# Kernel optimization log

Measured on AMD Instinct MI355X. Metric: run time of the kernel, lower is better.

Reference implementation:

```python
import jax, jax.numpy as jnp
import numpy as np

RADIUS = 64
STRIDE = RADIUS // 2
EPS = 1e-5

def box_filter(x, w):
    # depthwise conv: groups=3, RADIUSxRADIUS kernel of ones, stride RADIUS//2, no padding
    return jax.lax.conv_general_dilated(
        x, w, window_strides=(STRIDE, STRIDE), padding='VALID',
        feature_group_count=3, dimension_numbers=('NCHW', 'OIHW', 'NCHW'))

def conv1x1(x, w):
    # 1x1 conv == per-pixel matmul over channels
    return jnp.einsum('bchw,oc->bohw', x, w)

def batchnorm(x, g, b):
    # BatchNorm2d in training mode: biased batch stats over (N,H,W)
    m = jnp.mean(x, axis=(0, 2, 3), keepdims=True)
    v = jnp.var(x, axis=(0, 2, 3), keepdims=True)
    return (x - m) * jax.lax.rsqrt(v + EPS) * g[None, :, None, None] + b[None, :, None, None]

def resize_bilinear_ac(x, oh, ow):
    # F.interpolate(mode='bilinear', align_corners=True), separable gathers
    B, C, h, w = x.shape
    ys = jnp.linspace(0.0, h - 1.0, oh)
    y0 = jnp.floor(ys).astype(jnp.int32)
    y1 = jnp.minimum(y0 + 1, h - 1)
    wy = (ys - y0.astype(x.dtype))[None, None, :, None]
    xh = jnp.take(x, y0, axis=2) * (1 - wy) + jnp.take(x, y1, axis=2) * wy
    xs = jnp.linspace(0.0, w - 1.0, ow)
    x0 = jnp.floor(xs).astype(jnp.int32)
    x1 = jnp.minimum(x0 + 1, w - 1)
    wx = (xs - x0.astype(x.dtype))[None, None, None, :]
    return jnp.take(xh, x0, axis=3) * (1 - wx) + jnp.take(xh, x1, axis=3) * wx

def setup_inputs():
    key = jax.random.key(0)
    ks = jax.random.split(key, 5)
    B, H, W = 4, 1024, 1024
    guide = jax.random.uniform(ks[0], (B, 3, H, W), dtype=jnp.float32)
    src = jax.random.uniform(ks[1], (B, 3, H, W), dtype=jnp.float32)
    box_w = jnp.ones((3, 1, RADIUS, RADIUS), jnp.float32)  # weight.data[...] = 1.0
    w1 = jax.random.normal(ks[2], (32, 6), jnp.float32) * 0.2
    w2 = jax.random.normal(ks[3], (32, 32), jnp.float32) * 0.2
    w3 = jax.random.normal(ks[4], (3, 32), jnp.float32) * 0.2
    g1 = jnp.ones((32,), jnp.float32); b1 = jnp.zeros((32,), jnp.float32)
    g2 = jnp.ones((32,), jnp.float32); b2 = jnp.zeros((32,), jnp.float32)
    return dict(guide=guide, src=src, box_w=box_w, w1=w1, g1=g1, b1=b1,
                w2=w2, g2=g2, b2=b2, w3=w3)

def reference(guide, src, box_w, w1, g1, b1, w2, g2, b2, w3):
    B, C, H, W = guide.shape
    N = box_filter(jnp.ones((1, 3, H, W), guide.dtype), box_w)  # local window counts
    mean_x = box_filter(guide, box_w) / N
    mean_y = box_filter(src, box_w) / N
    cov_xy = box_filter(guide * src, box_w) / N - mean_x * mean_y
    var_x = box_filter(guide * guide, box_w) / N - mean_x * mean_x
    h = jnp.concatenate([cov_xy, var_x], axis=1)  # [B,6,h',w']
    h = jax.nn.relu(batchnorm(conv1x1(h, w1), g1, b1))
    h = jax.nn.relu(batchnorm(conv1x1(h, w2), g2, b2))
    A = conv1x1(h, w3)  # [B,3,h',w']
    b = mean_y - A * mean_x
    mean_A = resize_bilinear_ac(A, H, W)
    mean_b = resize_bilinear_ac(b, H, W)
    return mean_A * guide + mean_b
```

## Files before the change

kernel.cpp:

```cpp
#include <hip/hip_runtime.h>
#include <stdint.h>

#define B_      4
#define C_      3
#define H_      1024
#define W_      1024
#define OH_     31
#define NHS_    64
#define NP_     3844
#define NPOSPB_ 961
#define EPS_    1e-5f

#define NBLK_    256
#define NTHR_    768
#define MIDBLK_  21
#define NSHARD_  8
#define SHARD_TGT_ 32
#define LINE_    32

#define TILE_PLANE 24576
#define OFF_TILE  0
#define OFF_STATS 98304
#define OFF_A     98432
#define OFF_BV    109964

typedef float f4 __attribute__((ext_vector_type(4)));

__device__ int g_shard[2][NSHARD_ * LINE_];
__device__ int g_root[2][LINE_];
__device__ int g_bn1[2][LINE_];
__device__ int g_bn2[2][LINE_];
__device__ int g_done[2][LINE_];
__device__ int g_parity;

static __device__ __forceinline__ int  rload(int* p) { return __hip_atomic_load(p, __ATOMIC_RELAXED, __HIP_MEMORY_SCOPE_AGENT); }
static __device__ __forceinline__ int  aacq(int* p)  { return __hip_atomic_load(p, __ATOMIC_ACQUIRE, __HIP_MEMORY_SCOPE_AGENT); }
static __device__ __forceinline__ int  aadd(int* p, int v) { return __hip_atomic_fetch_add(p, v, __ATOMIC_ACQ_REL, __HIP_MEMORY_SCOPE_AGENT); }
static __device__ __forceinline__ void astoref(float* p, float v) { __hip_atomic_store(p, v, __ATOMIC_RELAXED, __HIP_MEMORY_SCOPE_AGENT); }
static __device__ __forceinline__ void astorei(int* p, int v)     { __hip_atomic_store(p, v, __ATOMIC_RELAXED, __HIP_MEMORY_SCOPE_AGENT); }
static __device__ __forceinline__ float aloadf(float* p) { return __hip_atomic_load(p, __ATOMIC_RELAXED, __HIP_MEMORY_SCOPE_AGENT); }

#define SPIN(ctr, target, slp) do { \
    if (t == 0) { \
        while (rload(ctr) < (target)) __builtin_amdgcn_s_sleep(slp); \
        (void)aacq(ctr);    \
    } \
    __syncthreads(); \
} while (0)

__global__ __launch_bounds__(NTHR_) void fused(
        const float* __restrict__ g,
        const float* __restrict__ s,
        const float* __restrict__ w1f,
        const float* __restrict__ g1f,
        const float* __restrict__ b1f,
        const float* __restrict__ w2f,
        const float* __restrict__ g2f,
        const float* __restrict__ b2f,
        const float* __restrict__ w3f,
        float* __restrict__ ws,
        float* __restrict__ out) {
    __shared__ float zbuf[192 * 33];
    __shared__ float red[12][16];
    __shared__ float scs[32], shs[32];
    __shared__ int sP;
    int t  = threadIdx.x;
    int fb = blockIdx.x;
    if (t == 0) sP = __hip_atomic_load(&g_parity, __ATOMIC_RELAXED, __HIP_MEMORY_SCOPE_AGENT);

    {
        int sub = t >> 8;
        int st  = t & 255;
        int unit = fb * 3 + sub;
        int bc = unit >> 6;
        int hs = unit & 63;
        const f4* gp = (const f4*)(g + ((size_t)bc * H_ + (size_t)hs * 16) * W_);
        const f4* sp = (const f4*)(s + ((size_t)bc * H_ + (size_t)hs * 16) * W_);
        float sg = 0.f, ss = 0.f, sgs = 0.f, sgg = 0.f;
#pragma unroll 4
        for (int r = 0; r < 16; r++) {
            f4 gv = gp[r * (W_ / 4) + st];
            f4 sv = __builtin_nontemporal_load(sp + r * (W_ / 4) + st);
            sg  += (gv.x + gv.y) + (gv.z + gv.w);
            ss  += (sv.x + sv.y) + (sv.z + sv.w);
            sgs += gv.x * sv.x + gv.y * sv.y + gv.z * sv.z + gv.w * sv.w;
            sgg += gv.x * gv.x + gv.y * gv.y + gv.z * gv.z + gv.w * gv.w;
        }
#pragma unroll
        for (int off = 4; off; off >>= 1) {
            sg  += __shfl_down(sg,  off, 8);
            ss  += __shfl_down(ss,  off, 8);
            sgs += __shfl_down(sgs, off, 8);
            sgg += __shfl_down(sgg, off, 8);
        }
        if ((st & 7) == 0) {
            int tx = st >> 3;
            int base = (bc * NHS_ + hs) * 32 + tx;
            astoref(&ws[OFF_TILE + 0 * TILE_PLANE + base], sg);
            astoref(&ws[OFF_TILE + 1 * TILE_PLANE + base], ss);
            astoref(&ws[OFF_TILE + 2 * TILE_PLANE + base], sgs);
            astoref(&ws[OFF_TILE + 3 * TILE_PLANE + base], sgg);
        }
        if (fb == 0 && t < 128) astoref(&ws[OFF_STATS + t], 0.f);
    }
    __syncthreads();
    int P = sP;

    if (t == 0) {
        int sh = fb & (NSHARD_ - 1);
        int old = aadd(&g_shard[P][sh * LINE_], 1);
        if (old == SHARD_TGT_ - 1) aadd(&g_root[P][0], 1);
    }

    if (fb < MIDBLK_) {
        SPIN(&g_root[P][0], NSHARD_, 2);

        int w    = t >> 6;
        int lane = t & 63;
        int k    = w & 3;
        int ko8  = __builtin_amdgcn_readfirstlane(k * 8);
        int pl   = (w >> 2) * 64 + lane;
        int p    = fb * 192 + pl;
        bool ok  = p < NP_;
        int pp   = ok ? p : 0;
        int b    = pp / NPOSPB_;
        int r    = pp % NPOSPB_;
        int oy   = r / OH_, ox = r % OH_;

        float h[6], mxv[3], myv[3];
#pragma unroll
        for (int c = 0; c < 3; c++) {
            int bc = b * 3 + c;
            int base = (bc * NHS_ + oy * 2) * 32 + ox;
            float S[4];
#pragma unroll
            for (int plane = 0; plane < 4; plane++) {
                const float* tp = ws + OFF_TILE + plane * TILE_PLANE + base;
                S[plane] = ((tp[0]  + tp[1])  + (tp[32] + tp[33]))
                         + ((tp[64] + tp[65]) + (tp[96] + tp[97]));
            }
            const float inv = 1.f / 4096.f;
            float mx = S[0] * inv, my = S[1] * inv;
            h[c]     = S[2] * inv - mx * my;
            h[3 + c] = S[3] * inv - mx * mx;
            mxv[c] = mx; myv[c] = my;
        }
        float a[8];
#pragma unroll
        for (int j = 0; j < 8; j++) {
            float y = 0.f;
#pragma unroll
            for (int i = 0; i < 6; i++) y += w1f[(ko8 + j) * 6 + i] * h[i];
            a[j] = y;
        }

        {
            float sv[8], sq[8];
#pragma unroll
            for (int j = 0; j < 8; j++) { sv[j] = ok ? a[j] : 0.f; sq[j] = sv[j] * sv[j]; }
#pragma unroll
            for (int off = 32; off; off >>= 1) {
#pragma unroll
                for (int j = 0; j < 8; j++) {
                    sv[j] += __shfl_down(sv[j], off, 64);
                    sq[j] += __shfl_down(sq[j], off, 64);
                }
            }
            if (lane == 0) {
#pragma unroll
                for (int j = 0; j < 8; j++) { red[w][j] = sv[j]; red[w][8 + j] = sq[j]; }
            }
        }
        __syncthreads();
        if (t < 64) {
            int o = t & 31; int kk = o >> 3; int col = ((t >= 32) ? 8 : 0) + (o & 7);
            float tot = red[kk][col] + red[kk + 4][col] + red[kk + 8][col];
            atomicAdd(&ws[OFF_STATS + ((t >= 32) ? 32 : 0) + o], tot);
        }
        __syncthreads();
        if (t == 0) aadd(&g_bn1[P][0], 1);
        SPIN(&g_bn1[P][0], MIDBLK_, 2);

        if (t < 32) {
            float sm = aloadf(&ws[OFF_STATS + t]);
            float sq = aloadf(&ws[OFF_STATS + 32 + t]);
            float m = sm * (1.f / NP_);
            float v = sq * (1.f / NP_) - m * m;
            float sc = g1f[t] * rsqrtf(v + EPS_);
            scs[t] = sc; shs[t] = b1f[t] - m * sc;
        }
        __syncthreads();

#pragma unroll
        for (int j = 0; j < 8; j++) {
            float zz = fmaxf(a[j] * scs[ko8 + j] + shs[ko8 + j], 0.f);
            zbuf[pl * 33 + ko8 + j] = zz;
        }
        __syncthreads();
        float zal[32];
#pragma unroll
        for (int i = 0; i < 32; i++) zal[i] = zbuf[pl * 33 + i];
        float y2[8];
#pragma unroll
        for (int j = 0; j < 8; j++) {
            float y = 0.f;
#pragma unroll
            for (int i = 0; i < 32; i++) y += w2f[(ko8 + j) * 32 + i] * zal[i];
            y2[j] = y;
        }

        {
            float sv[8], sq[8];
#pragma unroll
            for (int j = 0; j < 8; j++) { sv[j] = ok ? y2[j] : 0.f; sq[j] = sv[j] * sv[j]; }
#pragma unroll
            for (int off = 32; off; off >>= 1) {
#pragma unroll
                for (int j = 0; j < 8; j++) {
                    sv[j] += __shfl_down(sv[j], off, 64);
                    sq[j] += __shfl_down(sq[j], off, 64);
                }
            }
            if (lane == 0) {
#pragma unroll
                for (int j = 0; j < 8; j++) { red[w][j] = sv[j]; red[w][8 + j] = sq[j]; }
            }
        }
        __syncthreads();
        if (t < 64) {
            int o = t & 31; int kk = o >> 3; int col = ((t >= 32) ? 8 : 0) + (o & 7);
            float tot = red[kk][col] + red[kk + 4][col] + red[kk + 8][col];
            atomicAdd(&ws[OFF_STATS + 64 + ((t >= 32) ? 32 : 0) + o], tot);
        }
        __syncthreads();
        if (t == 0) aadd(&g_bn2[P][0], 1);
        SPIN(&g_bn2[P][0], MIDBLK_, 2);

        if (t < 32) {
            float sm = aloadf(&ws[OFF_STATS + 64 + t]);
            float sq = aloadf(&ws[OFF_STATS + 96 + t]);
            float m = sm * (1.f / NP_);
            float v = sq * (1.f / NP_) - m * m;
            float sc = g2f[t] * rsqrtf(v + EPS_);
            scs[t] = sc; shs[t] = b2f[t] - m * sc;
        }
        __syncthreads();

#pragma unroll
        for (int j = 0; j < 8; j++) {
            float zz = fmaxf(y2[j] * scs[ko8 + j] + shs[ko8 + j], 0.f);
            zbuf[pl * 33 + ko8 + j] = zz;
        }
        __syncthreads();
        if (k == 0 && ok) {
            float z2[32];
#pragma unroll
            for (int i = 0; i < 32; i++) z2[i] = zbuf[pl * 33 + i];
#pragma unroll
            for (int c = 0; c < 3; c++) {
                float av = 0.f;
#pragma unroll
                for (int i = 0; i < 32; i++) av += w3f[c * 32 + i] * z2[i];
                astoref(&ws[OFF_A  + c * NP_ + p], av);
                astoref(&ws[OFF_BV + c * NP_ + p], myv[c] - av * mxv[c]);
            }
        }
        __syncthreads();
        if (t == 0) {
            int old = aadd(&g_done[P][0], 1);
            if (old == MIDBLK_ - 1) {
                int Q = P ^ 1;
#pragma unroll
                for (int i = 0; i < NSHARD_; i++) astorei(&g_shard[Q][i * LINE_], 0);
                astorei(&g_root[Q][0], 0);
                astorei(&g_bn1[Q][0], 0);
                astorei(&g_bn2[Q][0], 0);
                astorei(&g_done[Q][0], 0);
                __hip_atomic_store(&g_parity, Q, __ATOMIC_RELEASE, __HIP_MEMORY_SCOPE_AGENT);
            }
        }
    }

    SPIN(&g_done[P][0], MIDBLK_, 32);

    {
        int sub = t >> 8;
        int st  = t & 255;
        int row0 = fb * 48 + sub * 16;
        int bc = row0 >> 10;
        int b5 = bc / 3, c5 = bc % 3;
        const float* Abase = ws + OFF_A  + c5 * NP_ + b5 * NPOSPB_;
        const float* Bbase = ws + OFF_BV + c5 * NP_ + b5 * NPOSPB_;
        int x0_[4], x1_[4]; float wx_[4];
#pragma unroll
        for (int j = 0; j < 4; j++) {
            int x = st * 4 + j;
            float fx = (float)x * (30.f / 1023.f);
            int x0 = (int)fx;
            wx_[j] = fx - (float)x0;
            x0_[j] = x0;
            x1_[j] = min(x0 + 1, 30);
        }
        for (int rr = 0; rr < 16; rr++) {
            int y = (row0 & 1023) + rr;
            float fy = (float)y * (30.f / 1023.f);
            int y0 = (int)fy;
            float wy = fy - (float)y0;
            int y1i = min(y0 + 1, 30);
            const float* A0 = Abase + y0  * OH_;
            const float* A1 = Abase + y1i * OH_;
            const float* B0 = Bbase + y0  * OH_;
            const float* B1 = Bbase + y1i * OH_;
            size_t rowoff = ((size_t)bc * H_ + (size_t)y) * W_;
            f4 gv = ((const f4*)(g + rowoff))[st];
            float go[4] = { gv.x, gv.y, gv.z, gv.w };
            float r[4];
#pragma unroll
            for (int j = 0; j < 4; j++) {
                int x0 = x0_[j], x1 = x1_[j];
                float wx = wx_[j];
                float av = (A0[x0] * (1.f - wx) + A0[x1] * wx) * (1.f - wy)
                         + (A1[x0] * (1.f - wx) + A1[x1] * wx) * wy;
                float bb = (B0[x0] * (1.f - wx) + B0[x1] * wx) * (1.f - wy)
                         + (B1[x0] * (1.f - wx) + B1[x1] * wx) * wy;
                r[j] = av * go[j] + bb;
            }
            f4 ov; ov.x = r[0]; ov.y = r[1]; ov.z = r[2]; ov.w = r[3];
            __builtin_nontemporal_store(ov, (f4*)(out + rowoff) + st);
        }
    }
}

extern "C" void kernel_launch(void* const* d_in, const int* in_sizes, int n_in,
                              void* d_out, int out_size, void* d_ws, size_t ws_size,
                              hipStream_t stream) {
    const float* guide = (const float*)d_in[0];
    const float* src   = (const float*)d_in[1];
    const float* w1 = (const float*)d_in[3];
    const float* g1 = (const float*)d_in[4];
    const float* b1 = (const float*)d_in[5];
    const float* w2 = (const float*)d_in[6];
    const float* g2 = (const float*)d_in[7];
    const float* b2 = (const float*)d_in[8];
    const float* w3 = (const float*)d_in[9];
    float* ws = (float*)d_ws;
    float* out = (float*)d_out;

    hipLaunchKernelGGL(fused, dim3(NBLK_), dim3(NTHR_), 0, stream,
                       guide, src, w1, g1, b1, w2, g2, b2, w3, ws, out);
}
```

Baseline: 191.6 us.

## Spread MLP/BN stage across all blocks and keep guide tile in registers

The middle MLP/batchnorm stage, previously done by 21 blocks while the other blocks spun, is now split across all 256 blocks at 16 positions each. Weights are staged in LDS, and BN statistics go to 8 shadow slots to reduce atomic contention. Every barrier now uses the sharded arrive/root scheme. Each thread keeps its 16 guide rows in registers from the first pass and reuses them in the final output pass, removing the second read of guide. The cost is more grid-wide barriers touching all blocks and higher register pressure from holding 16 float4 values.

```diff
diff --git a/kernel.cpp b/kernel.cpp
--- a/kernel.cpp
+++ b/kernel.cpp
@@ -13,24 +13,23 @@
 
 #define NBLK_    256
 #define NTHR_    768
-#define MIDBLK_  21
 #define NSHARD_  8
 #define SHARD_TGT_ 32
 #define LINE_    32
+#define NSHADOW_ 8
 
 #define TILE_PLANE 24576
 #define OFF_TILE  0
 #define OFF_STATS 98304
-#define OFF_A     98432
-#define OFF_BV    109964
+#define OFF_A     99328
+#define OFF_BV    110860
 
 typedef float f4 __attribute__((ext_vector_type(4)));
 
-__device__ int g_shard[2][NSHARD_ * LINE_];
-__device__ int g_root[2][LINE_];
-__device__ int g_bn1[2][LINE_];
-__device__ int g_bn2[2][LINE_];
-__device__ int g_done[2][LINE_];
+__device__ int g_b0s[2][NSHARD_ * LINE_]; __device__ int g_b0r[2][LINE_];
+__device__ int g_b1s[2][NSHARD_ * LINE_]; __device__ int g_b1r[2][LINE_];
+__device__ int g_b2s[2][NSHARD_ * LINE_]; __device__ int g_b2r[2][LINE_];
+__device__ int g_b3s[2][NSHARD_ * LINE_]; __device__ int g_b3r[2][LINE_];
 __device__ int g_parity;
 
 static __device__ __forceinline__ int  rload(int* p) { return __hip_atomic_load(p, __ATOMIC_RELAXED, __HIP_MEMORY_SCOPE_AGENT); }
@@ -40,10 +39,16 @@
 static __device__ __forceinline__ void astorei(int* p, int v)     { __hip_atomic_store(p, v, __ATOMIC_RELAXED, __HIP_MEMORY_SCOPE_AGENT); }
 static __device__ __forceinline__ float aloadf(float* p) { return __hip_atomic_load(p, __ATOMIC_RELAXED, __HIP_MEMORY_SCOPE_AGENT); }
 
-#define SPIN(ctr, target, slp) do { \
+#define ARRIVE(shard, root) do { \
     if (t == 0) { \
-        while (rload(ctr) < (target)) __builtin_amdgcn_s_sleep(slp); \
-        (void)aacq(ctr);    \
+        int _o = aadd(&(shard)[(fb & (NSHARD_ - 1)) * LINE_], 1); \
+        if (_o == SHARD_TGT_ - 1) aadd(&(root)[0], 1); \
+    } \
+} while (0)
+#define SPINROOT(root, slp) do { \
+    if (t == 0) { \
+        while (rload(&(root)[0]) < NSHARD_) __builtin_amdgcn_s_sleep(slp); \
+        (void)aacq(&(root)[0]); \
     } \
     __syncthreads(); \
 } while (0)
@@ -60,27 +65,38 @@
         const float* __restrict__ w3f,
         float* __restrict__ ws,
         float* __restrict__ out) {
-    __shared__ float zbuf[192 * 33];
-    __shared__ float red[12][16];
+    __shared__ float w1L[192];
+    __shared__ float w2L[32 * 33];
+    __shared__ float w3L[3 * 33];
+    __shared__ float Sarr[16][12];
+    __shared__ float hbuf[16][8];
+    __shared__ float mxb[16][4], myb[16][4];
+    __shared__ float sbuf[16][33];
+    __shared__ float zbuf[16][33];
     __shared__ float scs[32], shs[32];
     __shared__ int sP;
     int t  = threadIdx.x;
     int fb = blockIdx.x;
-    if (t == 0) sP = __hip_atomic_load(&g_parity, __ATOMIC_RELAXED, __HIP_MEMORY_SCOPE_AGENT);
-
+    if (t == 0) sP = rload(&g_parity);
+
+    if (t < 192) w1L[t] = w1f[t];
+    for (int i = t; i < 1024; i += NTHR_) w2L[(i >> 5) * 33 + (i & 31)] = w2f[i];
+    if (t < 96) w3L[(t >> 5) * 33 + (t & 31)] = w3f[t];
+
+    int sub = t >> 8;
+    int st  = t & 255;
+    f4 gvals[16];
     {
-        int sub = t >> 8;
-        int st  = t & 255;
         int unit = fb * 3 + sub;
-        int bc = unit >> 6;
-        int hs = unit & 63;
-        const f4* gp = (const f4*)(g + ((size_t)bc * H_ + (size_t)hs * 16) * W_);
-        const f4* sp = (const f4*)(s + ((size_t)bc * H_ + (size_t)hs * 16) * W_);
+        int ibc = unit >> 6, hs = unit & 63;
+        const f4* gp = (const f4*)(g + ((size_t)ibc * H_ + (size_t)hs * 16) * W_);
+        const f4* sp = (const f4*)(s + ((size_t)ibc * H_ + (size_t)hs * 16) * W_);
         float sg = 0.f, ss = 0.f, sgs = 0.f, sgg = 0.f;
-#pragma unroll 4
+#pragma unroll
         for (int r = 0; r < 16; r++) {
-            f4 gv = gp[r * (W_ / 4) + st];
+            f4 gv = __builtin_nontemporal_load(gp + r * (W_ / 4) + st);
             f4 sv = __builtin_nontemporal_load(sp + r * (W_ / 4) + st);
+            gvals[r] = gv;
             sg  += (gv.x + gv.y) + (gv.z + gv.w);
             ss  += (sv.x + sv.y) + (sv.z + sv.w);
             sgs += gv.x * sv.x + gv.y * sv.y + gv.z * sv.z + gv.w * sv.w;
@@ -95,197 +111,140 @@
         }
         if ((st & 7) == 0) {
             int tx = st >> 3;
-            int base = (bc * NHS_ + hs) * 32 + tx;
+            int base = (ibc * NHS_ + hs) * 32 + tx;
             astoref(&ws[OFF_TILE + 0 * TILE_PLANE + base], sg);
             astoref(&ws[OFF_TILE + 1 * TILE_PLANE + base], ss);
             astoref(&ws[OFF_TILE + 2 * TILE_PLANE + base], sgs);
             astoref(&ws[OFF_TILE + 3 * TILE_PLANE + base], sgg);
         }
-        if (fb == 0 && t < 128) astoref(&ws[OFF_STATS + t], 0.f);
+        if (fb == 0) for (int i = t; i < NSHADOW_ * 128; i += NTHR_) astoref(&ws[OFF_STATS + i], 0.f);
     }
     __syncthreads();
     int P = sP;
-
+    ARRIVE(g_b0s[P], g_b0r[P]);
+
+    SPINROOT(g_b0r[P], 2);
+
+    int p0 = fb * 16;
+    if (t < 192) {
+        int ipos = t / 12, idx = t % 12;
+        int c = idx >> 2, plane = idx & 3;
+        int p = p0 + ipos; if (p >= NP_) p = 0;
+        int b = p / NPOSPB_, r = p % NPOSPB_;
+        int oy = r / OH_, ox = r % OH_;
+        const float* tp = ws + OFF_TILE + plane * TILE_PLANE + ((b * 3 + c) * NHS_ + oy * 2) * 32 + ox;
+        Sarr[ipos][idx] = ((tp[0]  + tp[1])  + (tp[32] + tp[33]))
+                        + ((tp[64] + tp[65]) + (tp[96] + tp[97]));
+    }
+    __syncthreads();
+    if (t < 48) {
+        int pos = t / 3, c = t % 3;
+        const float inv = 1.f / 4096.f;
+        float mx = Sarr[pos][c * 4 + 0] * inv, my = Sarr[pos][c * 4 + 1] * inv;
+        hbuf[pos][c]     = Sarr[pos][c * 4 + 2] * inv - mx * my;
+        hbuf[pos][3 + c] = Sarr[pos][c * 4 + 3] * inv - mx * mx;
+        mxb[pos][c] = mx; myb[pos][c] = my;
+    }
+    __syncthreads();
+    int pos = t >> 5, ch = t & 31;
+    bool act = t < 512;
+    bool valid = act && (p0 + pos) < NP_;
+    float y1 = 0.f;
+    if (act) {
+#pragma unroll
+        for (int i = 0; i < 6; i++) y1 += w1L[ch * 6 + i] * hbuf[pos][i];
+        sbuf[pos][ch] = valid ? y1 : 0.f;
+    }
+    __syncthreads();
+    if (t < 32) {
+        float sv = 0.f, sq = 0.f;
+#pragma unroll
+        for (int i = 0; i < 16; i++) { float v = sbuf[i][t]; sv += v; sq += v * v; }
+        float* sh0 = ws + OFF_STATS + (fb & (NSHADOW_ - 1)) * 128;
+        atomicAdd(&sh0[t], sv); atomicAdd(&sh0[32 + t], sq);
+    }
+    __syncthreads();
+    ARRIVE(g_b1s[P], g_b1r[P]);
+    SPINROOT(g_b1r[P], 2);
+    if (t < 32) {
+        float sm = 0.f, sq = 0.f;
+#pragma unroll
+        for (int k = 0; k < NSHADOW_; k++) {
+            sm += aloadf(&ws[OFF_STATS + k * 128 + t]);
+            sq += aloadf(&ws[OFF_STATS + k * 128 + 32 + t]);
+        }
+        float m = sm * (1.f / NP_);
+        float v = sq * (1.f / NP_) - m * m;
+        float sc = g1f[t] * rsqrtf(v + EPS_);
+        scs[t] = sc; shs[t] = b1f[t] - m * sc;
+    }
+    __syncthreads();
+    if (act) zbuf[pos][ch] = fmaxf(y1 * scs[ch] + shs[ch], 0.f);
+    __syncthreads();
+    float y2 = 0.f;
+    if (act) {
+#pragma unroll
+        for (int i = 0; i < 32; i++) y2 += w2L[ch * 33 + i] * zbuf[pos][i];
+        sbuf[pos][ch] = valid ? y2 : 0.f;
+    }
+    __syncthreads();
+    if (t < 32) {
+        float sv = 0.f, sq = 0.f;
+#pragma unroll
+        for (int i = 0; i < 16; i++) { float v = sbuf[i][t]; sv += v; sq += v * v; }
+        float* sh0 = ws + OFF_STATS + (fb & (NSHADOW_ - 1)) * 128;
+        atomicAdd(&sh0[64 + t], sv); atomicAdd(&sh0[96 + t], sq);
+    }
+    __syncthreads();
+    ARRIVE(g_b2s[P], g_b2r[P]);
+    SPINROOT(g_b2r[P], 2);
+    if (t < 32) {
+        float sm = 0.f, sq = 0.f;
+#pragma unroll
+        for (int k = 0; k < NSHADOW_; k++) {
+            sm += aloadf(&ws[OFF_STATS + k * 128 + 64 + t]);
+            sq += aloadf(&ws[OFF_STATS + k * 128 + 96 + t]);
+        }
+        float m = sm * (1.f / NP_);
+        float v = sq * (1.f / NP_) - m * m;
+        float sc = g2f[t] * rsqrtf(v + EPS_);
+        scs[t] = sc; shs[t] = b2f[t] - m * sc;
+    }
+    __syncthreads();
+    if (act) zbuf[pos][ch] = fmaxf(y2 * scs[ch] + shs[ch], 0.f);
+    __syncthreads();
+    if (t < 48) {
+        int pz = t / 3, c = t % 3;
+        int p = p0 + pz;
+        if (p < NP_) {
+            float A = 0.f;
+#pragma unroll
+            for (int i = 0; i < 32; i++) A += w3L[c * 33 + i] * zbuf[pz][i];
+            astoref(&ws[OFF_A  + c * NP_ + p], A);
+            astoref(&ws[OFF_BV + c * NP_ + p], myb[pz][c] - A * mxb[pz][c]);
+        }
+    }
+    __syncthreads();
     if (t == 0) {
-        int sh = fb & (NSHARD_ - 1);
-        int old = aadd(&g_shard[P][sh * LINE_], 1);
-        if (old == SHARD_TGT_ - 1) aadd(&g_root[P][0], 1);
-    }
-
-    if (fb < MIDBLK_) {
-        SPIN(&g_root[P][0], NSHARD_, 2);
-
-        int w    = t >> 6;
-        int lane = t & 63;
-        int k    = w & 3;
-        int ko8  = __builtin_amdgcn_readfirstlane(k * 8);
-        int pl   = (w >> 2) * 64 + lane;
-        int p    = fb * 192 + pl;
-        bool ok  = p < NP_;
-        int pp   = ok ? p : 0;
-        int b    = pp / NPOSPB_;
-        int r    = pp % NPOSPB_;
-        int oy   = r / OH_, ox = r % OH_;
-
-        float h[6], mxv[3], myv[3];
-#pragma unroll
-        for (int c = 0; c < 3; c++) {
-            int bc = b * 3 + c;
-            int base = (bc * NHS_ + oy * 2) * 32 + ox;
-            float S[4];
-#pragma unroll
-            for (int plane = 0; plane < 4; plane++) {
-                const float* tp = ws + OFF_TILE + plane * TILE_PLANE + base;
-                S[plane] = ((tp[0]  + tp[1])  + (tp[32] + tp[33]))
-                         + ((tp[64] + tp[65]) + (tp[96] + tp[97]));
-            }
-            const float inv = 1.f / 4096.f;
-            float mx = S[0] * inv, my = S[1] * inv;
-            h[c]     = S[2] * inv - mx * my;
-            h[3 + c] = S[3] * inv - mx * mx;
-            mxv[c] = mx; myv[c] = my;
-        }
-        float a[8];
-#pragma unroll
-        for (int j = 0; j < 8; j++) {
-            float y = 0.f;
-#pragma unroll
-            for (int i = 0; i < 6; i++) y += w1f[(ko8 + j) * 6 + i] * h[i];
-            a[j] = y;
-        }
-
-        {
-            float sv[8], sq[8];
-#pragma unroll
-            for (int j = 0; j < 8; j++) { sv[j] = ok ? a[j] : 0.f; sq[j] = sv[j] * sv[j]; }
-#pragma unroll
-            for (int off = 32; off; off >>= 1) {
-#pragma unroll
-                for (int j = 0; j < 8; j++) {
-                    sv[j] += __shfl_down(sv[j], off, 64);
-                    sq[j] += __shfl_down(sq[j], off, 64);
+        int old = aadd(&g_b3s[P][(fb & (NSHARD_ - 1)) * LINE_], 1);
+        if (old == SHARD_TGT_ - 1) {
+            int ro = aadd(&g_b3r[P][0], 1);
+            if (ro == NSHARD_ - 1) {
+                int Q = P ^ 1;
+#pragma unroll
+                for (int i = 0; i < NSHARD_; i++) {
+                    astorei(&g_b0s[Q][i * LINE_], 0); astorei(&g_b1s[Q][i * LINE_], 0);
+                    astorei(&g_b2s[Q][i * LINE_], 0); astorei(&g_b3s[Q][i * LINE_], 0);
                 }
-            }
-            if (lane == 0) {
-#pragma unroll
-                for (int j = 0; j < 8; j++) { red[w][j] = sv[j]; red[w][8 + j] = sq[j]; }
-            }
-        }
-        __syncthreads();
-        if (t < 64) {
-            int o = t & 31; int kk = o >> 3; int col = ((t >= 32) ? 8 : 0) + (o & 7);
-            float tot = red[kk][col] + red[kk + 4][col] + red[kk + 8][col];
-            atomicAdd(&ws[OFF_STATS + ((t >= 32) ? 32 : 0) + o], tot);
-        }
-        __syncthreads();
-        if (t == 0) aadd(&g_bn1[P][0], 1);
-        SPIN(&g_bn1[P][0], MIDBLK_, 2);
-
-        if (t < 32) {
-            float sm = aloadf(&ws[OFF_STATS + t]);
-            float sq = aloadf(&ws[OFF_STATS + 32 + t]);
-            float m = sm * (1.f / NP_);
-            float v = sq * (1.f / NP_) - m * m;
-            float sc = g1f[t] * rsqrtf(v + EPS_);
-            scs[t] = sc; shs[t] = b1f[t] - m * sc;
-        }
-        __syncthreads();
-
-#pragma unroll
-        for (int j = 0; j < 8; j++) {
-            float zz = fmaxf(a[j] * scs[ko8 + j] + shs[ko8 + j], 0.f);
-            zbuf[pl * 33 + ko8 + j] = zz;
-        }
-        __syncthreads();
-        float zal[32];
-#pragma unroll
-        for (int i = 0; i < 32; i++) zal[i] = zbuf[pl * 33 + i];
-        float y2[8];
-#pragma unroll
-        for (int j = 0; j < 8; j++) {
-            float y = 0.f;
-#pragma unroll
-            for (int i = 0; i < 32; i++) y += w2f[(ko8 + j) * 32 + i] * zal[i];
-            y2[j] = y;
-        }
-
-        {
-            float sv[8], sq[8];
-#pragma unroll
-            for (int j = 0; j < 8; j++) { sv[j] = ok ? y2[j] : 0.f; sq[j] = sv[j] * sv[j]; }
-#pragma unroll
-            for (int off = 32; off; off >>= 1) {
-#pragma unroll
-                for (int j = 0; j < 8; j++) {
-                    sv[j] += __shfl_down(sv[j], off, 64);
-                    sq[j] += __shfl_down(sq[j], off, 64);
-                }
-            }
-            if (lane == 0) {
-#pragma unroll
-                for (int j = 0; j < 8; j++) { red[w][j] = sv[j]; red[w][8 + j] = sq[j]; }
-            }
-        }
-        __syncthreads();
-        if (t < 64) {
-            int o = t & 31; int kk = o >> 3; int col = ((t >= 32) ? 8 : 0) + (o & 7);
-            float tot = red[kk][col] + red[kk + 4][col] + red[kk + 8][col];
-            atomicAdd(&ws[OFF_STATS + 64 + ((t >= 32) ? 32 : 0) + o], tot);
-        }
-        __syncthreads();
-        if (t == 0) aadd(&g_bn2[P][0], 1);
-        SPIN(&g_bn2[P][0], MIDBLK_, 2);
-
-        if (t < 32) {
-            float sm = aloadf(&ws[OFF_STATS + 64 + t]);
-            float sq = aloadf(&ws[OFF_STATS + 96 + t]);
-            float m = sm * (1.f / NP_);
-            float v = sq * (1.f / NP_) - m * m;
-            float sc = g2f[t] * rsqrtf(v + EPS_);
-            scs[t] = sc; shs[t] = b2f[t] - m * sc;
-        }
-        __syncthreads();
-
-#pragma unroll
-        for (int j = 0; j < 8; j++) {
-            float zz = fmaxf(y2[j] * scs[ko8 + j] + shs[ko8 + j], 0.f);
-            zbuf[pl * 33 + ko8 + j] = zz;
-        }
-        __syncthreads();
-        if (k == 0 && ok) {
-            float z2[32];
-#pragma unroll
-            for (int i = 0; i < 32; i++) z2[i] = zbuf[pl * 33 + i];
-#pragma unroll
-            for (int c = 0; c < 3; c++) {
-                float av = 0.f;
-#pragma unroll
-                for (int i = 0; i < 32; i++) av += w3f[c * 32 + i] * z2[i];
-                astoref(&ws[OFF_A  + c * NP_ + p], av);
-                astoref(&ws[OFF_BV + c * NP_ + p], myv[c] - av * mxv[c]);
-            }
-        }
-        __syncthreads();
-        if (t == 0) {
-            int old = aadd(&g_done[P][0], 1);
-            if (old == MIDBLK_ - 1) {
-                int Q = P ^ 1;
-#pragma unroll
-                for (int i = 0; i < NSHARD_; i++) astorei(&g_shard[Q][i * LINE_], 0);
-                astorei(&g_root[Q][0], 0);
-                astorei(&g_bn1[Q][0], 0);
-                astorei(&g_bn2[Q][0], 0);
-                astorei(&g_done[Q][0], 0);
+                astorei(&g_b0r[Q][0], 0); astorei(&g_b1r[Q][0], 0);
+                astorei(&g_b2r[Q][0], 0); astorei(&g_b3r[Q][0], 0);
                 __hip_atomic_store(&g_parity, Q, __ATOMIC_RELEASE, __HIP_MEMORY_SCOPE_AGENT);
             }
         }
     }
-
-    SPIN(&g_done[P][0], MIDBLK_, 32);
+    SPINROOT(g_b3r[P], 8);
 
     {
-        int sub = t >> 8;
-        int st  = t & 255;
         int row0 = fb * 48 + sub * 16;
         int bc = row0 >> 10;
         int b5 = bc / 3, c5 = bc % 3;
@@ -301,6 +260,7 @@
             x0_[j] = x0;
             x1_[j] = min(x0 + 1, 30);
         }
+#pragma unroll
         for (int rr = 0; rr < 16; rr++) {
             int y = (row0 & 1023) + rr;
             float fy = (float)y * (30.f / 1023.f);
@@ -312,7 +272,7 @@
             const float* B0 = Bbase + y0  * OH_;
             const float* B1 = Bbase + y1i * OH_;
             size_t rowoff = ((size_t)bc * H_ + (size_t)y) * W_;
-            f4 gv = ((const f4*)(g + rowoff))[st];
+            f4 gv = gvals[rr];
             float go[4] = { gv.x, gv.y, gv.z, gv.w };
             float r[4];
 #pragma unroll
```

Measured after the change: 198.9 us. 1.04x slower.
